# Optimization experiments

Hardware: AMD Instinct MI355X
Metric: run time of the kernel (lower is better)

The kernel has to match this reference:

```python
import jax, jax.numpy as jnp
import numpy as np

D = 2048  # input_size
H = 2048  # hidden_size
K = 4096  # number of children


def setup_inputs() -> dict:
    key = jax.random.key(0)
    ks = jax.random.split(key, 12)
    sD = 1.0 / np.sqrt(D)
    sH = 1.0 / np.sqrt(H)
    return {
        "input": jax.random.normal(ks[0], (D,), dtype=jnp.float32),
        "children_c": jax.random.normal(ks[1], (K, H), dtype=jnp.float32),
        "children_h": jax.random.normal(ks[2], (K, H), dtype=jnp.float32),
        "W_iou_x": jax.random.uniform(ks[3], (3 * H, D), jnp.float32, -sD, sD),
        "b_iou_x": jax.random.uniform(ks[4], (3 * H,), jnp.float32, -sD, sD),
        "W_iou_h": jax.random.uniform(ks[5], (3 * H, H), jnp.float32, -sH, sH),
        "b_iou_h": jax.random.uniform(ks[6], (3 * H,), jnp.float32, -sH, sH),
        "W_fx": jax.random.uniform(ks[7], (H, D), jnp.float32, -sD, sD),
        "b_fx": jax.random.uniform(ks[8], (H,), jnp.float32, -sD, sD),
        "W_fh": jax.random.uniform(ks[9], (H, H), jnp.float32, -sH, sH),
        "b_fh": jax.random.uniform(ks[10], (H,), jnp.float32, -sH, sH),
    }


def reference(input, children_c, children_h,
              W_iou_x, b_iou_x, W_iou_h, b_iou_h,
              W_fx, b_fx, W_fh, b_fh):
    # iou = iou_x(input) + iou_h(sum_k h_k)  -> [3H]
    h_sum = jnp.sum(children_h, axis=0)
    iou = (W_iou_x @ input + b_iou_x) + (W_iou_h @ h_sum + b_iou_h)
    i, o, u = jnp.split(iou, 3)
    i = jax.nn.sigmoid(i)
    o = jax.nn.sigmoid(o)
    u = jnp.tanh(u)
    # per-child forget gates, batched over K (original loops in Python):
    # f_k = sigmoid(f_x(input) + f_h(h_k))  -> [K, H]
    fx = W_fx @ input + b_fx                       # [H], computed once
    fh = children_h @ W_fh.T + b_fh                # [K, H] GEMM
    f = jax.nn.sigmoid(fx[None, :] + fh)           # [K, H]
    c = i * u + jnp.sum(f * children_c, axis=0)    # [H]
    h = o * jnp.tanh(c)                            # [H]
    return (o, c, h)
```

## Files before the change

kernel.cpp:

```cpp
#include <hip/hip_runtime.h>

typedef unsigned short u16;
typedef short bf16x8 __attribute__((ext_vector_type(8)));
typedef float f32x4 __attribute__((ext_vector_type(4)));

#define D_IN 2048
#define H_DIM 2048
#define K_CH 4096

__device__ __forceinline__ u16 f2bf(float f) {
  unsigned int u = __float_as_uint(f);
  u += 0x7fffu + ((u >> 16) & 1u);
  return (u16)(u >> 16);
}
__device__ __forceinline__ float sigmoidf(float x) {
  return 1.0f / (1.0f + __expf(-x));
}
__device__ __forceinline__ uint4 packrow(float4 a, float4 b) {
  uint4 w;
  w.x = (unsigned)f2bf(a.x) | ((unsigned)f2bf(a.y) << 16);
  w.y = (unsigned)f2bf(a.z) | ((unsigned)f2bf(a.w) << 16);
  w.z = (unsigned)f2bf(b.x) | ((unsigned)f2bf(b.y) << 16);
  w.w = (unsigned)f2bf(b.z) | ((unsigned)f2bf(b.w) << 16);
  return w;
}

__global__ __launch_bounds__(256) void kprep(const float* __restrict__ ch,
                                             const float* __restrict__ wfh,
                                             float* __restrict__ partials,
                                             u16* __restrict__ chb,
                                             u16* __restrict__ wfhb) {
  const int t = threadIdx.x;
  if (blockIdx.x < 1024) {
    const int r0 = blockIdx.x * 4;
    float4 a[4], b[4];
#pragma unroll
    for (int r = 0; r < 4; ++r) {
      const float4* p = (const float4*)(ch + (size_t)(r0 + r) * H_DIM + t * 8);
      a[r] = p[0];
      b[r] = p[1];
    }
    float s0 = 0.f, s1 = 0.f, s2 = 0.f, s3 = 0.f;
    float s4 = 0.f, s5 = 0.f, s6 = 0.f, s7 = 0.f;
#pragma unroll
    for (int r = 0; r < 4; ++r) {
      s0 += a[r].x; s1 += a[r].y; s2 += a[r].z; s3 += a[r].w;
      s4 += b[r].x; s5 += b[r].y; s6 += b[r].z; s7 += b[r].w;
      *(uint4*)(chb + (size_t)(r0 + r) * H_DIM + t * 8) = packrow(a[r], b[r]);
    }
    float4 lo, hi;
    lo.x = s0; lo.y = s1; lo.z = s2; lo.w = s3;
    hi.x = s4; hi.y = s5; hi.z = s6; hi.w = s7;
    float* pp = partials + (size_t)blockIdx.x * H_DIM + t * 8;
    *(float4*)pp = lo;
    *(float4*)(pp + 4) = hi;
  } else {
    const size_t base = (size_t)(blockIdx.x - 1024) * 8192 + t * 8;
    float4 a[4], b[4];
#pragma unroll
    for (int j = 0; j < 4; ++j) {
      const float4* p = (const float4*)(wfh + base + j * 2048);
      a[j] = p[0];
      b[j] = p[1];
    }
#pragma unroll
    for (int j = 0; j < 4; ++j)
      *(uint4*)(wfhb + base + j * 2048) = packrow(a[j], b[j]);
  }
}

__global__ __launch_bounds__(256) void kred(const float* __restrict__ partials,
                                            float* __restrict__ hsum) {
  const int c = blockIdx.x * 256 + threadIdx.x;
  const int p0 = blockIdx.y * 128;
  float a0 = 0.f, a1 = 0.f, a2 = 0.f, a3 = 0.f;
  float a4 = 0.f, a5 = 0.f, a6 = 0.f, a7 = 0.f;
  for (int p = p0; p < p0 + 128; p += 8) {
    a0 += partials[(size_t)(p + 0) * H_DIM + c];
    a1 += partials[(size_t)(p + 1) * H_DIM + c];
    a2 += partials[(size_t)(p + 2) * H_DIM + c];
    a3 += partials[(size_t)(p + 3) * H_DIM + c];
    a4 += partials[(size_t)(p + 4) * H_DIM + c];
    a5 += partials[(size_t)(p + 5) * H_DIM + c];
    a6 += partials[(size_t)(p + 6) * H_DIM + c];
    a7 += partials[(size_t)(p + 7) * H_DIM + c];
  }
  float s = ((a0 + a1) + (a2 + a3)) + ((a4 + a5) + (a6 + a7));
  atomicAdd(hsum + c, s);
}

__global__ __launch_bounds__(256) void kmatvec(
    const float* __restrict__ Wix, const float* __restrict__ bix,
    const float* __restrict__ Wih, const float* __restrict__ bih,
    const float* __restrict__ Wfx, const float* __restrict__ bfx,
    const float* __restrict__ bfh, const float* __restrict__ x,
    const float* __restrict__ hsum, float* __restrict__ iou,
    float* __restrict__ g) {
  const int wave = threadIdx.x >> 6, lane = threadIdx.x & 63;
  const int row = blockIdx.x * 4 + wave;
  float s = 0.f;
  if (row < 6144) {
    const float4* wx = (const float4*)(Wix + (size_t)row * D_IN);
    const float4* wh = (const float4*)(Wih + (size_t)row * H_DIM);
    const float4* xv = (const float4*)x;
    const float4* hv = (const float4*)hsum;
#pragma unroll
    for (int i = 0; i < 8; ++i) {
      int idx = i * 64 + lane;
      float4 a = wx[idx], b = xv[idx];
      s += a.x * b.x + a.y * b.y + a.z * b.z + a.w * b.w;
      float4 c = wh[idx], d = hv[idx];
      s += c.x * d.x + c.y * d.y + c.z * d.z + c.w * d.w;
    }
#pragma unroll
    for (int off = 32; off > 0; off >>= 1) s += __shfl_xor(s, off);
    if (lane == 0) iou[row] = s + bix[row] + bih[row];
  } else {
    const int h = row - 6144;
    const float4* w = (const float4*)(Wfx + (size_t)h * D_IN);
    const float4* xv = (const float4*)x;
#pragma unroll
    for (int i = 0; i < 8; ++i) {
      int idx = i * 64 + lane;
      float4 a = w[idx], b = xv[idx];
      s += a.x * b.x + a.y * b.y + a.z * b.z + a.w * b.w;
    }
#pragma unroll
    for (int off = 32; off > 0; off >>= 1) s += __shfl_xor(s, off);
    if (lane == 0) g[h] = s + bfx[h] + bfh[h];
  }
}

#define BM 128
#define BN 128
#define BK 64

__global__ __launch_bounds__(256) void kgemm(
    const u16* __restrict__ chb, const float* __restrict__ cc,
    const u16* __restrict__ wfhb, const float* __restrict__ g,
    float* __restrict__ accv) {
  __shared__ u16 As[BM * BK];
  __shared__ u16 Bs[BN * BK];

  const int t = threadIdx.x;
  const int wave = t >> 6, lane = t & 63;
  const int lrow = lane & 15, lquad = lane >> 4;
  const int wm = wave >> 1, wn = wave & 1;
  const int row0 = blockIdx.x * BM;
  const int col0 = blockIdx.y * BN;

  f32x4 acc[4][4] = {};

  const int srow = lane >> 3;
  const int schunk = (lane & 7) ^ srow;
  const u16* agbase = chb  + (size_t)(row0 + wave * 32 + srow) * H_DIM + schunk * 8;
  const u16* bgbase = wfhb + (size_t)(col0 + wave * 32 + srow) * H_DIM + schunk * 8;

  for (int kb = 0; kb < D_IN / BK; ++kb) {
    __syncthreads();
#pragma unroll
    for (int i = 0; i < 4; ++i)
      __builtin_amdgcn_global_load_lds(
          (const __attribute__((address_space(1))) void*)(agbase + (size_t)i * 8 * H_DIM + kb * BK),
          (__attribute__((address_space(3))) void*)(As + (wave * 32 + i * 8) * 64),
          16, 0, 0);
#pragma unroll
    for (int i = 0; i < 4; ++i)
      __builtin_amdgcn_global_load_lds(
          (const __attribute__((address_space(1))) void*)(bgbase + (size_t)i * 8 * H_DIM + kb * BK),
          (__attribute__((address_space(3))) void*)(Bs + (wave * 32 + i * 8) * 64),
          16, 0, 0);
    __syncthreads();

#pragma unroll
    for (int step = 0; step < 2; ++step) {
      const int slot = ((step * 4 + lquad) ^ (lrow & 7)) * 8;
      bf16x8 fa[4], fb[4];
#pragma unroll
      for (int i = 0; i < 4; ++i)
        fa[i] = *(const bf16x8*)(As + (wm * 64 + i * 16 + lrow) * 64 + slot);
#pragma unroll
      for (int i = 0; i < 4; ++i)
        fb[i] = *(const bf16x8*)(Bs + (wn * 64 + i * 16 + lrow) * 64 + slot);
#pragma unroll
      for (int mi = 0; mi < 4; ++mi)
#pragma unroll
        for (int ni = 0; ni < 4; ++ni)
          acc[mi][ni] = __builtin_amdgcn_mfma_f32_16x16x32_bf16(
              fa[mi], fb[ni], acc[mi][ni], 0, 0, 0);
    }
  }

#pragma unroll
  for (int ni = 0; ni < 4; ++ni) {
    const int colg = col0 + wn * 64 + ni * 16 + lrow;
    const float gv = g[colg];
    float s = 0.f;
#pragma unroll
    for (int mi = 0; mi < 4; ++mi) {
      const int rowg = row0 + wm * 64 + mi * 16 + lquad * 4;
#pragma unroll
      for (int r = 0; r < 4; ++r) {
        float f = sigmoidf(gv + acc[mi][ni][r]);
        s += f * cc[(size_t)(rowg + r) * H_DIM + colg];
      }
    }
    s += __shfl_xor(s, 16);
    s += __shfl_xor(s, 32);
    if (lquad == 0) atomicAdd(accv + colg, s);
  }
}

__global__ __launch_bounds__(256) void kfinal(const float* __restrict__ iou,
                                              const float* __restrict__ accv,
                                              float* __restrict__ out) {
  const int h = blockIdx.x * 256 + threadIdx.x;
  float si = sigmoidf(iou[h]);
  float so = sigmoidf(iou[H_DIM + h]);
  float tu = tanhf(iou[2 * H_DIM + h]);
  float c = si * tu + accv[h];
  float hh = so * tanhf(c);
  out[h] = so;
  out[H_DIM + h] = c;
  out[2 * H_DIM + h] = hh;
}

extern "C" void kernel_launch(void* const* d_in, const int* in_sizes, int n_in,
                              void* d_out, int out_size, void* d_ws, size_t ws_size,
                              hipStream_t stream) {
  const float* x   = (const float*)d_in[0];
  const float* cc  = (const float*)d_in[1];
  const float* ch  = (const float*)d_in[2];
  const float* Wix = (const float*)d_in[3];
  const float* bix = (const float*)d_in[4];
  const float* Wih = (const float*)d_in[5];
  const float* bih = (const float*)d_in[6];
  const float* Wfx = (const float*)d_in[7];
  const float* bfx = (const float*)d_in[8];
  const float* Wfh = (const float*)d_in[9];
  const float* bfh = (const float*)d_in[10];

  float* ws   = (float*)d_ws;
  float* hsum = ws;
  float* iou  = ws + 2048;
  float* g    = ws + 8192;
  float* accv = ws + 10240;
  float* partials = ws + 12288;
  u16* chb  = (u16*)(ws + 12288 + 1024 * 2048);
  u16* wfhb = chb + (size_t)K_CH * H_DIM;
  float* out = (float*)d_out;

  hipMemsetAsync(ws, 0, 12288 * sizeof(float), stream);
  kprep<<<1536, 256, 0, stream>>>(ch, Wfh, partials, chb, wfhb);
  kred<<<dim3(8, 8), 256, 0, stream>>>(partials, hsum);
  kmatvec<<<2048, 256, 0, stream>>>(Wix, bix, Wih, bih, Wfx, bfx, bfh, x, hsum, iou, g);
  kgemm<<<dim3(32, 16), 256, 0, stream>>>(chb, cc, wfhb, g, accv);
  kfinal<<<8, 256, 0, stream>>>(iou, accv, out);
}
```

Baseline: 280.9 us.

## Merge matvecs into prep and GEMM kernels, replace memset with in-kernel zeroing

Moves the W_fx matvec (forget-gate bias) into the prep kernel and zeroes hsum/accv from an extra block there, which removes the memset launch. The iou matvec now runs as extra blocks inside the GEMM kernel so the two overlap, and the separate matvec launch is gone. This cuts launch count and lets bandwidth-bound matvec work fill idle CUs beside the 512 GEMM blocks. The cost is that the GEMM blocks still allocate LDS that the matvec blocks never use, which may limit occupancy for those blocks.

Result: faster. 271.8 us (-3.3%).

```diff
diff --git a/kernel.cpp b/kernel.cpp
--- a/kernel.cpp
+++ b/kernel.cpp
@@ -25,14 +25,17 @@
   return w;
 }
 
-__global__ __launch_bounds__(256) void kprep(const float* __restrict__ ch,
-                                             const float* __restrict__ wfh,
-                                             float* __restrict__ partials,
-                                             u16* __restrict__ chb,
-                                             u16* __restrict__ wfhb) {
+__global__ __launch_bounds__(256) void k1(
+    const float* __restrict__ ch, const float* __restrict__ wfh,
+    const float* __restrict__ Wfx, const float* __restrict__ bfx,
+    const float* __restrict__ bfh, const float* __restrict__ x,
+    float* __restrict__ partials, u16* __restrict__ chb,
+    u16* __restrict__ wfhb, float* __restrict__ g,
+    float* __restrict__ hsum, float* __restrict__ accv) {
   const int t = threadIdx.x;
-  if (blockIdx.x < 1024) {
-    const int r0 = blockIdx.x * 4;
+  const int bid = blockIdx.x;
+  if (bid < 1024) {
+    const int r0 = bid * 4;
     float4 a[4], b[4];
 #pragma unroll
     for (int r = 0; r < 4; ++r) {
@@ -51,11 +54,11 @@
     float4 lo, hi;
     lo.x = s0; lo.y = s1; lo.z = s2; lo.w = s3;
     hi.x = s4; hi.y = s5; hi.z = s6; hi.w = s7;
-    float* pp = partials + (size_t)blockIdx.x * H_DIM + t * 8;
+    float* pp = partials + (size_t)bid * H_DIM + t * 8;
     *(float4*)pp = lo;
     *(float4*)(pp + 4) = hi;
-  } else {
-    const size_t base = (size_t)(blockIdx.x - 1024) * 8192 + t * 8;
+  } else if (bid < 1536) {
+    const size_t base = (size_t)(bid - 1024) * 8192 + t * 8;
     float4 a[4], b[4];
 #pragma unroll
     for (int j = 0; j < 4; ++j) {
@@ -66,6 +69,27 @@
 #pragma unroll
     for (int j = 0; j < 4; ++j)
       *(uint4*)(wfhb + base + j * 2048) = packrow(a[j], b[j]);
+  } else if (bid < 2048) {
+    const int wave = t >> 6, lane = t & 63;
+    const int h = (bid - 1536) * 4 + wave;
+    const float4* w = (const float4*)(Wfx + (size_t)h * D_IN);
+    const float4* xv = (const float4*)x;
+    float s = 0.f;
+#pragma unroll
+    for (int i = 0; i < 8; ++i) {
+      int idx = i * 64 + lane;
+      float4 av = w[idx], bv = xv[idx];
+      s += av.x * bv.x + av.y * bv.y + av.z * bv.z + av.w * bv.w;
+    }
+#pragma unroll
+    for (int off = 32; off > 0; off >>= 1) s += __shfl_xor(s, off);
+    if (lane == 0) g[h] = s + bfx[h] + bfh[h];
+  } else {
+    float4 z = {0.f, 0.f, 0.f, 0.f};
+    ((float4*)hsum)[t * 2] = z;
+    ((float4*)hsum)[t * 2 + 1] = z;
+    ((float4*)accv)[t * 2] = z;
+    ((float4*)accv)[t * 2 + 1] = z;
   }
 }
 
@@ -89,21 +113,97 @@
   atomicAdd(hsum + c, s);
 }
 
-__global__ __launch_bounds__(256) void kmatvec(
-    const float* __restrict__ Wix, const float* __restrict__ bix,
-    const float* __restrict__ Wih, const float* __restrict__ bih,
-    const float* __restrict__ Wfx, const float* __restrict__ bfx,
-    const float* __restrict__ bfh, const float* __restrict__ x,
-    const float* __restrict__ hsum, float* __restrict__ iou,
-    float* __restrict__ g) {
-  const int wave = threadIdx.x >> 6, lane = threadIdx.x & 63;
-  const int row = blockIdx.x * 4 + wave;
-  float s = 0.f;
-  if (row < 6144) {
+#define BM 128
+#define BN 128
+#define BK 64
+
+__global__ __launch_bounds__(256) void k3(
+    const u16* __restrict__ chb, const float* __restrict__ cc,
+    const u16* __restrict__ wfhb, const float* __restrict__ g,
+    float* __restrict__ accv, const float* __restrict__ Wix,
+    const float* __restrict__ bix, const float* __restrict__ Wih,
+    const float* __restrict__ bih, const float* __restrict__ x,
+    const float* __restrict__ hsum, float* __restrict__ iou) {
+  __shared__ u16 As[BM * BK];
+  __shared__ u16 Bs[BN * BK];
+
+  const int bid = blockIdx.x;
+  const int t = threadIdx.x;
+  const int wave = t >> 6, lane = t & 63;
+
+  if (bid < 512) {
+    const int lrow = lane & 15, lquad = lane >> 4;
+    const int wm = wave >> 1, wn = wave & 1;
+    const int row0 = (bid & 31) * BM;
+    const int col0 = (bid >> 5) * BN;
+
+    f32x4 acc[4][4] = {};
+
+    const int srow = lane >> 3;
+    const int schunk = (lane & 7) ^ srow;
+    const u16* agbase = chb  + (size_t)(row0 + wave * 32 + srow) * H_DIM + schunk * 8;
+    const u16* bgbase = wfhb + (size_t)(col0 + wave * 32 + srow) * H_DIM + schunk * 8;
+
+    for (int kb = 0; kb < D_IN / BK; ++kb) {
+      __syncthreads();
+#pragma unroll
+      for (int i = 0; i < 4; ++i)
+        __builtin_amdgcn_global_load_lds(
+            (const __attribute__((address_space(1))) void*)(agbase + (size_t)i * 8 * H_DIM + kb * BK),
+            (__attribute__((address_space(3))) void*)(As + (wave * 32 + i * 8) * 64),
+            16, 0, 0);
+#pragma unroll
+      for (int i = 0; i < 4; ++i)
+        __builtin_amdgcn_global_load_lds(
+            (const __attribute__((address_space(1))) void*)(bgbase + (size_t)i * 8 * H_DIM + kb * BK),
+            (__attribute__((address_space(3))) void*)(Bs + (wave * 32 + i * 8) * 64),
+            16, 0, 0);
+      __syncthreads();
+
+#pragma unroll
+      for (int step = 0; step < 2; ++step) {
+        const int slot = ((step * 4 + lquad) ^ (lrow & 7)) * 8;
+        bf16x8 fa[4], fb[4];
+#pragma unroll
+        for (int i = 0; i < 4; ++i)
+          fa[i] = *(const bf16x8*)(As + (wm * 64 + i * 16 + lrow) * 64 + slot);
+#pragma unroll
+        for (int i = 0; i < 4; ++i)
+          fb[i] = *(const bf16x8*)(Bs + (wn * 64 + i * 16 + lrow) * 64 + slot);
+#pragma unroll
+        for (int mi = 0; mi < 4; ++mi)
+#pragma unroll
+          for (int ni = 0; ni < 4; ++ni)
+            acc[mi][ni] = __builtin_amdgcn_mfma_f32_16x16x32_bf16(
+                fa[mi], fb[ni], acc[mi][ni], 0, 0, 0);
+      }
+    }
+
+#pragma unroll
+    for (int ni = 0; ni < 4; ++ni) {
+      const int colg = col0 + wn * 64 + ni * 16 + lrow;
+      const float gv = g[colg];
+      float s = 0.f;
+#pragma unroll
+      for (int mi = 0; mi < 4; ++mi) {
+        const int rowg = row0 + wm * 64 + mi * 16 + lquad * 4;
+#pragma unroll
+        for (int r = 0; r < 4; ++r) {
+          float f = sigmoidf(gv + acc[mi][ni][r]);
+          s += f * cc[(size_t)(rowg + r) * H_DIM + colg];
+        }
+      }
+      s += __shfl_xor(s, 16);
+      s += __shfl_xor(s, 32);
+      if (lquad == 0) atomicAdd(accv + colg, s);
+    }
+  } else {
+    const int row = (bid - 512) * 4 + wave;
     const float4* wx = (const float4*)(Wix + (size_t)row * D_IN);
     const float4* wh = (const float4*)(Wih + (size_t)row * H_DIM);
     const float4* xv = (const float4*)x;
     const float4* hv = (const float4*)hsum;
+    float s = 0.f;
 #pragma unroll
     for (int i = 0; i < 8; ++i) {
       int idx = i * 64 + lane;
@@ -115,99 +215,6 @@
 #pragma unroll
     for (int off = 32; off > 0; off >>= 1) s += __shfl_xor(s, off);
     if (lane == 0) iou[row] = s + bix[row] + bih[row];
-  } else {
-    const int h = row - 6144;
-    const float4* w = (const float4*)(Wfx + (size_t)h * D_IN);
-    const float4* xv = (const float4*)x;
-#pragma unroll
-    for (int i = 0; i < 8; ++i) {
-      int idx = i * 64 + lane;
-      float4 a = w[idx], b = xv[idx];
-      s += a.x * b.x + a.y * b.y + a.z * b.z + a.w * b.w;
-    }
-#pragma unroll
-    for (int off = 32; off > 0; off >>= 1) s += __shfl_xor(s, off);
-    if (lane == 0) g[h] = s + bfx[h] + bfh[h];
-  }
-}
-
-#define BM 128
-#define BN 128
-#define BK 64
-
-__global__ __launch_bounds__(256) void kgemm(
-    const u16* __restrict__ chb, const float* __restrict__ cc,
-    const u16* __restrict__ wfhb, const float* __restrict__ g,
-    float* __restrict__ accv) {
-  __shared__ u16 As[BM * BK];
-  __shared__ u16 Bs[BN * BK];
-
-  const int t = threadIdx.x;
-  const int wave = t >> 6, lane = t & 63;
-  const int lrow = lane & 15, lquad = lane >> 4;
-  const int wm = wave >> 1, wn = wave & 1;
-  const int row0 = blockIdx.x * BM;
-  const int col0 = blockIdx.y * BN;
-
-  f32x4 acc[4][4] = {};
-
-  const int srow = lane >> 3;
-  const int schunk = (lane & 7) ^ srow;
-  const u16* agbase = chb  + (size_t)(row0 + wave * 32 + srow) * H_DIM + schunk * 8;
-  const u16* bgbase = wfhb + (size_t)(col0 + wave * 32 + srow) * H_DIM + schunk * 8;
-
-  for (int kb = 0; kb < D_IN / BK; ++kb) {
-    __syncthreads();
-#pragma unroll
-    for (int i = 0; i < 4; ++i)
-      __builtin_amdgcn_global_load_lds(
-          (const __attribute__((address_space(1))) void*)(agbase + (size_t)i * 8 * H_DIM + kb * BK),
-          (__attribute__((address_space(3))) void*)(As + (wave * 32 + i * 8) * 64),
-          16, 0, 0);
-#pragma unroll
-    for (int i = 0; i < 4; ++i)
-      __builtin_amdgcn_global_load_lds(
-          (const __attribute__((address_space(1))) void*)(bgbase + (size_t)i * 8 * H_DIM + kb * BK),
-          (__attribute__((address_space(3))) void*)(Bs + (wave * 32 + i * 8) * 64),
-          16, 0, 0);
-    __syncthreads();
-
-#pragma unroll
-    for (int step = 0; step < 2; ++step) {
-      const int slot = ((step * 4 + lquad) ^ (lrow & 7)) * 8;
-      bf16x8 fa[4], fb[4];
-#pragma unroll
-      for (int i = 0; i < 4; ++i)
-        fa[i] = *(const bf16x8*)(As + (wm * 64 + i * 16 + lrow) * 64 + slot);
-#pragma unroll
-      for (int i = 0; i < 4; ++i)
-        fb[i] = *(const bf16x8*)(Bs + (wn * 64 + i * 16 + lrow) * 64 + slot);
-#pragma unroll
-      for (int mi = 0; mi < 4; ++mi)
-#pragma unroll
-        for (int ni = 0; ni < 4; ++ni)
-          acc[mi][ni] = __builtin_amdgcn_mfma_f32_16x16x32_bf16(
-              fa[mi], fb[ni], acc[mi][ni], 0, 0, 0);
-    }
-  }
-
-#pragma unroll
-  for (int ni = 0; ni < 4; ++ni) {
-    const int colg = col0 + wn * 64 + ni * 16 + lrow;
-    const float gv = g[colg];
-    float s = 0.f;
-#pragma unroll
-    for (int mi = 0; mi < 4; ++mi) {
-      const int rowg = row0 + wm * 64 + mi * 16 + lquad * 4;
-#pragma unroll
-      for (int r = 0; r < 4; ++r) {
-        float f = sigmoidf(gv + acc[mi][ni][r]);
-        s += f * cc[(size_t)(rowg + r) * H_DIM + colg];
-      }
-    }
-    s += __shfl_xor(s, 16);
-    s += __shfl_xor(s, 32);
-    if (lquad == 0) atomicAdd(accv + colg, s);
   }
 }
 
@@ -250,10 +257,8 @@
   u16* wfhb = chb + (size_t)K_CH * H_DIM;
   float* out = (float*)d_out;
 
-  hipMemsetAsync(ws, 0, 12288 * sizeof(float), stream);
-  kprep<<<1536, 256, 0, stream>>>(ch, Wfh, partials, chb, wfhb);
+  k1<<<2049, 256, 0, stream>>>(ch, Wfh, Wfx, bfx, bfh, x, partials, chb, wfhb, g, hsum, accv);
   kred<<<dim3(8, 8), 256, 0, stream>>>(partials, hsum);
-  kmatvec<<<2048, 256, 0, stream>>>(Wix, bix, Wih, bih, Wfx, bfx, bfh, x, hsum, iou, g);
-  kgemm<<<dim3(32, 16), 256, 0, stream>>>(chb, cc, wfhb, g, accv);
+  k3<<<2048, 256, 0, stream>>>(chb, cc, wfhb, g, accv, Wix, bix, Wih, bih, x, hsum, iou);
   kfinal<<<8, 256, 0, stream>>>(iou, accv, out);
 }
```
